# Kernel tuning notes

Hardware: AMD Instinct MI355X
Metric: run time of the kernel (lower is better)

The kernel has to match this reference:

```python
import jax, jax.numpy as jnp
import numpy as np
import math

B, L, D, H = 8, 2048, 1024, 1024


def setup_inputs() -> dict:
    key = jax.random.key(0)
    ks = jax.random.split(key, 6)
    scale = 1.0 / math.sqrt(D)
    return {
        "input_q": jax.random.normal(ks[0], (B, L, D), dtype=jnp.float32),
        "input_k": jax.random.normal(ks[1], (B, L, D), dtype=jnp.float32),
        "k_mask": jax.random.uniform(ks[2], (B, L), dtype=jnp.float32),
        "Wq": jax.random.normal(ks[3], (D, H), dtype=jnp.float32) * scale,
        "bq": jnp.zeros((H,), dtype=jnp.float32),
        "Wk": jax.random.normal(ks[4], (D, H), dtype=jnp.float32) * scale,
        "bk": jnp.zeros((H,), dtype=jnp.float32),
    }


def reference(input_q, input_k, k_mask, Wq, bq, Wk, bk):
    # Linear projections: (b, l, d) @ (d, h) -> (b, l, h)
    q = input_q @ Wq + bq
    k = input_k @ Wk + bk
    # Faithful to original: mask values become 0.0 or -1e9, then an
    # outer product bmm((b,l,1),(b,1,l)) builds the (b,l,l) additive mask.
    m = jnp.where(k_mask > 0.5, 0.0, -1000000000.0)  # (b, l)
    add_mask = m[:, :, None] * m[:, None, :]          # (b, l, l) outer product
    # Scaled dot-product scores
    attn = jnp.einsum("bqh,bkh->bqk", q, k) / math.sqrt(H)
    attn = jax.nn.softmax(attn + add_mask, axis=-1)
    # Weighted sum over the ORIGINAL input_k (not projected k), as in source
    out = jnp.einsum("bqk,bkd->bqd", attn, input_k)
    return out
```

## Files before the change

kernel.cpp:

```cpp
#include <hip/hip_runtime.h>

#define BATCH 8
#define SEQ   2048
#define DIM   1024

typedef __attribute__((ext_vector_type(8)))  short short8;
typedef __attribute__((ext_vector_type(4)))  short short4v;
typedef __attribute__((ext_vector_type(4)))  float floatx4;
typedef __attribute__((ext_vector_type(16))) float floatx16;

__device__ __forceinline__ unsigned short f32_to_bf16(float f) {
    union { float f; unsigned int u; } x; x.f = f;
    unsigned int r = x.u + 0x7fffu + ((x.u >> 16) & 1u);
    return (unsigned short)(r >> 16);
}

__device__ __forceinline__ float bf16_to_f32(unsigned short h) {
    union { unsigned int u; float f; } x; x.u = ((unsigned int)h) << 16;
    return x.f;
}

__device__ __forceinline__ void async_load16(const void* g, void* l) {
    __builtin_amdgcn_global_load_lds(
        (const __attribute__((address_space(1))) void*)g,
        (__attribute__((address_space(3))) void*)l, 16, 0, 0);
}

__global__ __launch_bounds__(256) void build_idx(
    const float* __restrict__ mask, int* __restrict__ idx,
    int* __restrict__ cnt, int* __restrict__ padcnt)
{
    const int b = blockIdx.x;
    const int t = threadIdx.x;
    const float* mb = mask + b * SEQ;
    int flags[8]; int c = 0;
#pragma unroll
    for (int j = 0; j < 8; ++j) {
        flags[j] = (mb[t * 8 + j] > 0.5f) ? 1 : 0;
        c += flags[j];
    }
    int sc = c;
    for (int o = 1; o < 64; o <<= 1) {
        int v = __shfl_up(sc, o);
        if ((t & 63) >= o) sc += v;
    }
    __shared__ int wtot[4];
    const int lane = t & 63, wave = t >> 6;
    if (lane == 63) wtot[wave] = sc;
    __syncthreads();
    int woff = 0;
    for (int w = 0; w < wave; ++w) woff += wtot[w];
    int p = woff + sc - c;
#pragma unroll
    for (int j = 0; j < 8; ++j)
        if (flags[j]) idx[b * SEQ + (p++)] = t * 8 + j;
    __syncthreads();
    const int total = wtot[0] + wtot[1] + wtot[2] + wtot[3];
    if (t == 0) { cnt[b] = total; padcnt[b] = (total + 127) & ~127; }
    for (int q = total + t; q < SEQ; q += 256) idx[b * SEQ + q] = 0;
}

__global__ __launch_bounds__(256) void gather_cvt_q(
    const float* __restrict__ xq, const int* __restrict__ idx,
    const int* __restrict__ padcnt, unsigned short* __restrict__ qc)
{
    const int b = blockIdx.y;
    const int rc = blockIdx.x;
    if (rc >= padcnt[b]) return;
    const int src = idx[b * SEQ + rc];
    const float* s = xq + ((long)b * SEQ + src) * DIM + threadIdx.x * 4;
    unsigned short* d = qc + ((long)b * SEQ + rc) * DIM + threadIdx.x * 4;
    floatx4 v = *(const floatx4*)s;
    short4v w;
#pragma unroll
    for (int j = 0; j < 4; ++j) w[j] = (short)f32_to_bf16(v[j]);
    *(short4v*)d = w;
}

__global__ __launch_bounds__(256) void prep_kv(
    const float* __restrict__ xk, const float* __restrict__ mask,
    unsigned short* __restrict__ kbf, unsigned short* __restrict__ Vt,
    float* __restrict__ mavg)
{
    __shared__ float tile[32][33];
    __shared__ float msk[32];
    __shared__ float csum[8][32];
    const int b  = blockIdx.z;
    const int c0 = blockIdx.x * 32;
    const int r0 = blockIdx.y * 32;
    const int tx = threadIdx.x & 31, ty = threadIdx.x >> 5;
    const float* xb = xk + (long)b * SEQ * DIM;
    unsigned short* kb = kbf + (long)b * SEQ * DIM;
    unsigned short* vb = Vt + (long)b * DIM * SEQ;

    if (threadIdx.x < 32) msk[threadIdx.x] = mask[b * SEQ + r0 + threadIdx.x];

    float v[4];
#pragma unroll
    for (int i = 0; i < 4; ++i) {
        const int r = ty + i * 8;
        v[i] = xb[(long)(r0 + r) * DIM + c0 + tx];
        tile[r][tx] = v[i];
        kb[(long)(r0 + r) * DIM + c0 + tx] = f32_to_bf16(v[i]);
    }
    __syncthreads();

    float s = 0.f;
#pragma unroll
    for (int i = 0; i < 4; ++i) {
        const int r = ty + i * 8;
        s += (msk[r] <= 0.5f) ? v[i] : 0.f;
    }
    csum[ty][tx] = s;

#pragma unroll
    for (int i = 0; i < 4; ++i) {
        const int c = ty + i * 8;
        vb[(long)(c0 + c) * SEQ + r0 + tx] = f32_to_bf16(tile[tx][c]);
    }
    __syncthreads();
    if (ty == 0) {
        float t = 0.f;
#pragma unroll
        for (int j = 0; j < 8; ++j) t += csum[j][tx];
        atomicAdd(&mavg[b * DIM + c0 + tx], t);
    }
}

__global__ __launch_bounds__(256) void cvt_bf16(
    const float* __restrict__ src, unsigned short* __restrict__ dst)
{
    const long i = ((long)blockIdx.x * 256 + threadIdx.x) * 8;
    floatx4 v0 = *(const floatx4*)(src + i);
    floatx4 v1 = *(const floatx4*)(src + i + 4);
    short8 w;
#pragma unroll
    for (int j = 0; j < 4; ++j) w[j]     = (short)f32_to_bf16(v0[j]);
#pragma unroll
    for (int j = 0; j < 4; ++j) w[4 + j] = (short)f32_to_bf16(v1[j]);
    *(short8*)(dst + i) = w;
}

__global__ __launch_bounds__(256) void proj_bias(
    const float* __restrict__ bq, const float* __restrict__ Wk, float* __restrict__ g0)
{
    const int n = blockIdx.x;
    const int t = threadIdx.x;
    float s = 0.f;
    for (int h = t; h < DIM; h += 256) s += bq[h] * Wk[(long)n * DIM + h];
    for (int o = 32; o; o >>= 1) s += __shfl_xor(s, o);
    __shared__ float r[4];
    if ((t & 63) == 0) r[t >> 6] = s;
    __syncthreads();
    if (t == 0) g0[n] = r[0] + r[1] + r[2] + r[3];
}

template<bool C_BF16, bool BIAS, bool LIMIT, bool SCATTER, int FLAT>
__global__ __launch_bounds__(256) void gemm_bt(
    const unsigned short* __restrict__ A, const unsigned short* __restrict__ Bt,
    void* __restrict__ Cp, const float* __restrict__ bias,
    int N, int K, long sA, long sB, long sC, float scale,
    const int* __restrict__ mlim, const int* __restrict__ cntp,
    const int* __restrict__ idx, int sh)
{
    int bx, by, bz;
    if (FLAT == 0) {
        bx = blockIdx.x; by = blockIdx.y; bz = blockIdx.z;
    } else {
        const int id = blockIdx.x;
        bz = id & 7;
        const int rem = id >> 3;
        const int m = (1 << sh) - 1;
        if (FLAT == 1) { bx = rem & m; by = rem >> sh; }
        else           { by = rem & m; bx = rem >> sh; }
    }
    const int row0 = bx * 128;
    if (LIMIT && row0 >= mlim[bz]) return;

    __shared__ unsigned short As[128 * 64];
    __shared__ unsigned short Bs[128 * 64];

    const int tid  = threadIdx.x;
    const int lane = tid & 63;
    const int wave = tid >> 6;
    const int wm   = wave >> 1;
    const int wn   = wave & 1;
    const int l31  = lane & 31;
    const int half = lane >> 5;
    const int x7   = lane & 7;
    const int col0 = by * 128;
    const long zA = (long)bz * sA;
    const long zB = (long)bz * sB;
    const long zC = (long)bz * sC;

    const int sr = lane >> 3;
    const int sq = ((lane & 7) ^ sr) * 8;

    const unsigned short* Abase = A  + zA + (long)row0 * K;
    const unsigned short* Bbase = Bt + zB + (long)col0 * K;
    const unsigned short* aptr[4];
    const unsigned short* bptr[4];
#pragma unroll
    for (int c = 0; c < 4; ++c) {
        const int r = (wave * 4 + c) * 8 + sr;
        aptr[c] = Abase + (long)r * K + sq;
        bptr[c] = Bbase + (long)r * K + sq;
    }

    floatx16 acc[2][2];
#pragma unroll
    for (int a = 0; a < 2; ++a)
#pragma unroll
        for (int b = 0; b < 2; ++b)
#pragma unroll
            for (int r = 0; r < 16; ++r) acc[a][b][r] = 0.f;

    const int raf[2] = { (wm * 64 +  0 + l31) * 64, (wm * 64 + 32 + l31) * 64 };
    const int rbf[2] = { (wn * 64 +  0 + l31) * 64, (wn * 64 + 32 + l31) * 64 };

    for (int kt = 0; kt < K; kt += 64) {
#pragma unroll
        for (int c = 0; c < 4; ++c) {
            const int chunk = wave * 4 + c;
            async_load16(aptr[c] + kt, As + chunk * 512);
            async_load16(bptr[c] + kt, Bs + chunk * 512);
        }
        __syncthreads();

#pragma unroll
        for (int ks = 0; ks < 4; ++ks) {
            const int sw = ((ks * 2 + half) ^ x7) << 3;
            short8 af[2], bf[2];
#pragma unroll
            for (int t = 0; t < 2; ++t) {
                af[t] = *(const short8*)(As + raf[t] + sw);
                bf[t] = *(const short8*)(Bs + rbf[t] + sw);
            }
#pragma unroll
            for (int tm = 0; tm < 2; ++tm)
#pragma unroll
                for (int tn = 0; tn < 2; ++tn)
                    acc[tm][tn] = __builtin_amdgcn_mfma_f32_32x32x16_bf16(
                        af[tm], bf[tn], acc[tm][tn], 0, 0, 0);
        }
        __syncthreads();
    }

    const int climit = SCATTER ? cntp[bz] : 0;
    const int* ridx  = SCATTER ? (idx + bz * SEQ) : (const int*)nullptr;
#pragma unroll
    for (int tn = 0; tn < 2; ++tn) {
        const int ccol = col0 + wn * 64 + tn * 32 + l31;
        float bv = 0.f;
        if (BIAS) bv = bias[ccol];
#pragma unroll
        for (int tm = 0; tm < 2; ++tm) {
            const int rbase = row0 + wm * 64 + tm * 32 + 4 * half;
#pragma unroll
            for (int r = 0; r < 16; ++r) {
                const int crow = rbase + (r & 3) + 8 * (r >> 2);
                float v = acc[tm][tn][r] * scale + bv;
                long orow = crow;
                if (SCATTER) {
                    if (crow >= climit) continue;
                    orow = ridx[crow];
                }
                const long ci = zC + orow * (long)N + ccol;
                if (C_BF16) ((unsigned short*)Cp)[ci] = f32_to_bf16(v);
                else        ((float*)Cp)[ci] = v;
            }
        }
    }
}

__global__ __launch_bounds__(256) void softmax_rows(
    unsigned short* __restrict__ S, const int* __restrict__ padcnt)
{
    const int b = blockIdx.x >> 11, rc = blockIdx.x & 2047;
    if (rc >= padcnt[b]) return;
    const long base = (long)blockIdx.x * SEQ + threadIdx.x * 8;
    const int lane = threadIdx.x & 63, wave = threadIdx.x >> 6;
    __shared__ float rbuf[8];

    short8 v = *(const short8*)(S + base);
    float x[8];
#pragma unroll
    for (int j = 0; j < 8; ++j) x[j] = bf16_to_f32((unsigned short)v[j]);

    float m = x[0];
#pragma unroll
    for (int j = 1; j < 8; ++j) m = fmaxf(m, x[j]);
    for (int o = 32; o; o >>= 1) m = fmaxf(m, __shfl_xor(m, o));
    if (lane == 0) rbuf[wave] = m;
    __syncthreads();
    m = fmaxf(fmaxf(rbuf[0], rbuf[1]), fmaxf(rbuf[2], rbuf[3]));

    float e[8], s = 0.f;
#pragma unroll
    for (int j = 0; j < 8; ++j) { e[j] = __expf(x[j] - m); s += e[j]; }
    for (int o = 32; o; o >>= 1) s += __shfl_xor(s, o);
    if (lane == 0) rbuf[4 + wave] = s;
    __syncthreads();
    s = rbuf[4] + rbuf[5] + rbuf[6] + rbuf[7];
    const float inv = 1.0f / s;

    short8 o8;
#pragma unroll
    for (int j = 0; j < 8; ++j) o8[j] = (short)f32_to_bf16(e[j] * inv);
    *(short8*)(S + base) = o8;
}

__global__ __launch_bounds__(256) void overwrite_masked(
    float* __restrict__ out, const float* __restrict__ mask,
    const float* __restrict__ mavg, const int* __restrict__ cnt)
{
    const int bid = blockIdx.x;
    const int b = bid >> 11;
    if (mask[bid] > 0.5f) return;
    const float inv = 1.0f / (float)(SEQ - cnt[b]);
    const long obase = (long)bid * DIM;
    const float* mv = mavg + b * DIM;
    for (int d = threadIdx.x; d < DIM; d += 256)
        out[obase + d] = mv[d] * inv;
}

extern "C" void kernel_launch(void* const* d_in, const int* in_sizes, int n_in,
                              void* d_out, int out_size, void* d_ws, size_t ws_size,
                              hipStream_t stream) {
    (void)in_sizes; (void)n_in; (void)out_size;
    const float* input_q = (const float*)d_in[0];
    const float* input_k = (const float*)d_in[1];
    const float* k_mask  = (const float*)d_in[2];
    const float* Wq      = (const float*)d_in[3];
    const float* bq      = (const float*)d_in[4];
    const float* Wk      = (const float*)d_in[5];
    const float* bk      = (const float*)d_in[6];
    (void)bk;
    float* out = (float*)d_out;

    char* ws = (char*)d_ws;
    unsigned short* qc   = (unsigned short*)(ws);
    unsigned short* S    = (unsigned short*)(ws);
    unsigned short* qpp  = (unsigned short*)(ws + 67108864);
    unsigned short* Wqb  = (unsigned short*)(ws + 67108864);
    unsigned short* Wkb  = (unsigned short*)(ws + 69206016);
    unsigned short* kbf  = (unsigned short*)(ws + 100663296);
    unsigned short* Vt   = (unsigned short*)(ws + 134217728);
    unsigned short* Gt   = (unsigned short*)(ws + 167772160);
    float*          g0   = (float*)(ws + 169869312);
    float*          mavg = (float*)(ws + 169873408);
    int*            idx  = (int*)(ws + 169906176);
    int*            cnts = (int*)(ws + 169971712);
    int*            pcnt = (int*)(ws + 169971744);
    if (ws_size < 169971776) return;

    hipMemsetAsync(mavg, 0, BATCH * DIM * sizeof(float), stream);

    build_idx<<<BATCH, 256, 0, stream>>>(k_mask, idx, cnts, pcnt);
    gather_cvt_q<<<dim3(SEQ, BATCH), 256, 0, stream>>>(input_q, idx, pcnt, qc);
    prep_kv<<<dim3(DIM / 32, SEQ / 32, BATCH), 256, 0, stream>>>(input_k, k_mask, kbf, Vt, mavg);
    cvt_bf16<<<512, 256, 0, stream>>>(Wq, Wqb);
    cvt_bf16<<<512, 256, 0, stream>>>(Wk, Wkb);
    proj_bias<<<DIM, 256, 0, stream>>>(bq, Wk, g0);

    gemm_bt<true, false, false, false, 0><<<dim3(8, 8, 1), 256, 0, stream>>>(
        Wkb, Wqb, Gt, nullptr, DIM, DIM, 0, 0, 0, 1.0f, nullptr, nullptr, nullptr, 0);

    gemm_bt<true, true, true, false, 2><<<8 * 16 * 8, 256, 0, stream>>>(
        qc, Gt, qpp, g0, DIM, DIM,
        (long)SEQ * DIM, 0, (long)SEQ * DIM, 1.0f, pcnt, nullptr, nullptr, 3);

    gemm_bt<true, false, true, false, 1><<<8 * 16 * 16, 256, 0, stream>>>(
        qpp, kbf, S, nullptr, SEQ, DIM,
        (long)SEQ * DIM, (long)SEQ * DIM, (long)SEQ * SEQ, 0.03125f, pcnt, nullptr, nullptr, 4);

    softmax_rows<<<BATCH * SEQ, 256, 0, stream>>>(S, pcnt);

    gemm_bt<false, false, true, true, 2><<<8 * 16 * 8, 256, 0, stream>>>(
        S, Vt, out, nullptr, DIM, SEQ,
        (long)SEQ * SEQ, (long)DIM * SEQ, (long)SEQ * DIM, 1.0f, pcnt, cnts, idx, 3);

    overwrite_masked<<<BATCH * SEQ, 256, 0, stream>>>(out, k_mask, mavg, cnts);
}
```

Baseline: 365.5 us.

## Double-buffer GEMM LDS tiles with async prefetch two stages ahead

Turns the single-buffer GEMM main loop into a two-slot LDS ping-pong. The global-to-LDS load for tile t+2 is issued right after the last fragment reads of tile t, and waits use explicit vmcnt/lgkmcnt counts with raw s_barrier instead of __syncthreads, so global latency overlaps with MFMA work. MFMA bursts run at raised wave priority via s_setprio. LDS use doubles to 64 KB per block, which may lower occupancy, and the hand-written waitcnt values must match the issued load count exactly.

Measured after the change: 401.5 us. 1.1x slower.

```diff
diff --git a/kernel.cpp b/kernel.cpp
--- a/kernel.cpp
+++ b/kernel.cpp
@@ -177,8 +177,8 @@
     const int row0 = bx * 128;
     if (LIMIT && row0 >= mlim[bz]) return;
 
-    __shared__ unsigned short As[128 * 64];
-    __shared__ unsigned short Bs[128 * 64];
+    __shared__ unsigned short As[2][128 * 64];
+    __shared__ unsigned short Bs[2][128 * 64];
 
     const int tid  = threadIdx.x;
     const int lane = tid & 63;
@@ -207,6 +207,15 @@
         bptr[c] = Bbase + (long)r * K + sq;
     }
 
+    auto stage = [&](int slot, int ktElem) {
+#pragma unroll
+        for (int c = 0; c < 4; ++c) {
+            const int chunk = wave * 4 + c;
+            async_load16(aptr[c] + ktElem, &As[slot][chunk * 512]);
+            async_load16(bptr[c] + ktElem, &Bs[slot][chunk * 512]);
+        }
+    };
+
     floatx16 acc[2][2];
 #pragma unroll
     for (int a = 0; a < 2; ++a)
@@ -218,32 +227,80 @@
     const int raf[2] = { (wm * 64 +  0 + l31) * 64, (wm * 64 + 32 + l31) * 64 };
     const int rbf[2] = { (wn * 64 +  0 + l31) * 64, (wn * 64 + 32 + l31) * 64 };
 
-    for (int kt = 0; kt < K; kt += 64) {
-#pragma unroll
-        for (int c = 0; c < 4; ++c) {
-            const int chunk = wave * 4 + c;
-            async_load16(aptr[c] + kt, As + chunk * 512);
-            async_load16(bptr[c] + kt, Bs + chunk * 512);
+    const int NT = K >> 6;
+
+    stage(0, 0);
+    if (NT > 1) {
+        stage(1, 64);
+        asm volatile("s_waitcnt vmcnt(8)" ::: "memory");
+    } else {
+        asm volatile("s_waitcnt vmcnt(0)" ::: "memory");
+    }
+    __builtin_amdgcn_sched_barrier(0);
+    __builtin_amdgcn_s_barrier();
+    __builtin_amdgcn_sched_barrier(0);
+
+    for (int t = 0; t < NT; ++t) {
+        const int cur = t & 1;
+        const unsigned short* Ac = &As[cur][0];
+        const unsigned short* Bc = &Bs[cur][0];
+
+        short8 af[2][2], bf[2][2];
+#pragma unroll
+        for (int ks = 0; ks < 2; ++ks) {
+            const int sw = ((ks * 2 + half) ^ x7) << 3;
+#pragma unroll
+            for (int tt = 0; tt < 2; ++tt) {
+                af[ks][tt] = *(const short8*)(Ac + raf[tt] + sw);
+                bf[ks][tt] = *(const short8*)(Bc + rbf[tt] + sw);
+            }
         }
-        __syncthreads();
-
-#pragma unroll
-        for (int ks = 0; ks < 4; ++ks) {
-            const int sw = ((ks * 2 + half) ^ x7) << 3;
-            short8 af[2], bf[2];
-#pragma unroll
-            for (int t = 0; t < 2; ++t) {
-                af[t] = *(const short8*)(As + raf[t] + sw);
-                bf[t] = *(const short8*)(Bs + rbf[t] + sw);
-            }
+        asm volatile("s_waitcnt lgkmcnt(0)" ::: "memory");
+        __builtin_amdgcn_sched_barrier(0);
+        __builtin_amdgcn_s_setprio(1);
+#pragma unroll
+        for (int ks = 0; ks < 2; ++ks)
 #pragma unroll
             for (int tm = 0; tm < 2; ++tm)
 #pragma unroll
                 for (int tn = 0; tn < 2; ++tn)
                     acc[tm][tn] = __builtin_amdgcn_mfma_f32_32x32x16_bf16(
-                        af[tm], bf[tn], acc[tm][tn], 0, 0, 0);
+                        af[ks][tm], bf[ks][tn], acc[tm][tn], 0, 0, 0);
+        __builtin_amdgcn_s_setprio(0);
+
+#pragma unroll
+        for (int ks = 0; ks < 2; ++ks) {
+            const int sw = (((ks + 2) * 2 + half) ^ x7) << 3;
+#pragma unroll
+            for (int tt = 0; tt < 2; ++tt) {
+                af[ks][tt] = *(const short8*)(Ac + raf[tt] + sw);
+                bf[ks][tt] = *(const short8*)(Bc + rbf[tt] + sw);
+            }
         }
-        __syncthreads();
+        asm volatile("s_waitcnt lgkmcnt(0)" ::: "memory");
+        __builtin_amdgcn_sched_barrier(0);
+        __builtin_amdgcn_s_barrier();
+        __builtin_amdgcn_sched_barrier(0);
+        if (t + 2 < NT) stage(cur, (t + 2) * 64);
+        __builtin_amdgcn_sched_barrier(0);
+        __builtin_amdgcn_s_setprio(1);
+#pragma unroll
+        for (int ks = 0; ks < 2; ++ks)
+#pragma unroll
+            for (int tm = 0; tm < 2; ++tm)
+#pragma unroll
+                for (int tn = 0; tn < 2; ++tn)
+                    acc[tm][tn] = __builtin_amdgcn_mfma_f32_32x32x16_bf16(
+                        af[ks][tm], bf[ks][tn], acc[tm][tn], 0, 0, 0);
+        __builtin_amdgcn_s_setprio(0);
+
+        if (t + 1 < NT) {
+            if (t + 2 < NT) asm volatile("s_waitcnt vmcnt(8)" ::: "memory");
+            else            asm volatile("s_waitcnt vmcnt(0)" ::: "memory");
+            __builtin_amdgcn_sched_barrier(0);
+            __builtin_amdgcn_s_barrier();
+            __builtin_amdgcn_sched_barrier(0);
+        }
     }
 
     const int climit = SCATTER ? cntp[bz] : 0;
```

## Add 256x256-tile 8-wave GEMM with double-buffered LDS ping-pong schedule

Applied to the files above, without the earlier changes.

Introduces a new gemm256 kernel using 256x256 output tiles, 512 threads, 128KB dynamic LDS with double buffering and a fine-grained barrier-interleaved schedule of LDS reads, async global-to-LDS loads and 16x16x32 bf16 MFMAs. The three large batched GEMMs (q projection, scores, and attention-times-V) switch from the 128-tile gemm_bt to this kernel. The aim is more data reuse per tile and better overlap of memory traffic with MFMA work. In exchange, grids are much smaller, so there are fewer blocks to spread across CUs, one block per CU because of LDS usage, and wave quantization and masked-row limits may leave CUs idle.

Result: slower. 401.7 us (+9.9%).

```diff
diff --git a/kernel.cpp b/kernel.cpp
--- a/kernel.cpp
+++ b/kernel.cpp
@@ -25,6 +25,11 @@
         (const __attribute__((address_space(1))) void*)g,
         (__attribute__((address_space(3))) void*)l, 16, 0, 0);
 }
+
+#define CFENCE asm volatile("" ::: "memory")
+#define BARF() do { CFENCE; __builtin_amdgcn_s_barrier(); CFENCE; } while (0)
+#define WAIT_LGKM0 do { asm volatile("s_waitcnt lgkmcnt(0)" ::: "memory"); \
+                        __builtin_amdgcn_sched_barrier(0); } while (0)
 
 __global__ __launch_bounds__(256) void build_idx(
     const float* __restrict__ mask, int* __restrict__ idx,
@@ -260,6 +265,232 @@
             for (int r = 0; r < 16; ++r) {
                 const int crow = rbase + (r & 3) + 8 * (r >> 2);
                 float v = acc[tm][tn][r] * scale + bv;
+                long orow = crow;
+                if (SCATTER) {
+                    if (crow >= climit) continue;
+                    orow = ridx[crow];
+                }
+                const long ci = zC + orow * (long)N + ccol;
+                if (C_BF16) ((unsigned short*)Cp)[ci] = f32_to_bf16(v);
+                else        ((float*)Cp)[ci] = v;
+            }
+        }
+    }
+}
+
+template<int D, int MQ>
+__device__ __forceinline__ void read_a256(short8 (&af)[4][2],
+                                          const unsigned short* const (&aB)[2][2]) {
+#pragma unroll
+    for (int mm = 0; mm < 4; ++mm)
+#pragma unroll
+        for (int ss = 0; ss < 2; ++ss)
+            af[mm][ss] = *(const short8*)(aB[D][ss] + (MQ * 64 + mm * 16) * 64);
+}
+
+template<int D, int NQ>
+__device__ __forceinline__ void read_b256(short8 (&bf)[2][2][2],
+                                          const unsigned short* const (&bB)[2][2]) {
+#pragma unroll
+    for (int nn = 0; nn < 2; ++nn)
+#pragma unroll
+        for (int ss = 0; ss < 2; ++ss)
+            bf[NQ][nn][ss] = *(const short8*)(bB[D][ss] + (NQ * 32 + nn * 16) * 64);
+}
+
+template<int MQ, int NQ>
+__device__ __forceinline__ void mfma_q256(floatx4 (&acc)[8][4],
+                                          const short8 (&af)[4][2],
+                                          const short8 (&bf)[2][2][2]) {
+    __builtin_amdgcn_s_setprio(1);
+#pragma unroll
+    for (int mm = 0; mm < 4; ++mm)
+#pragma unroll
+        for (int nn = 0; nn < 2; ++nn)
+#pragma unroll
+            for (int ss = 0; ss < 2; ++ss)
+                acc[MQ * 4 + mm][NQ * 2 + nn] = __builtin_amdgcn_mfma_f32_16x16x32_bf16(
+                    af[mm][ss], bf[NQ][nn][ss], acc[MQ * 4 + mm][NQ * 2 + nn], 0, 0, 0);
+    __builtin_amdgcn_s_setprio(0);
+}
+
+__device__ __forceinline__ void stage2(const unsigned short* s0, const unsigned short* s1,
+                                       unsigned short* d) {
+    async_load16(s0, d);
+    async_load16(s1, d + 512);
+}
+
+template<bool C_BF16, bool BIAS, bool LIMIT, bool SCATTER, int FLAT>
+__global__ __launch_bounds__(512) void gemm256(
+    const unsigned short* __restrict__ A, const unsigned short* __restrict__ Bt,
+    void* __restrict__ Cp, const float* __restrict__ bias,
+    int N, int K, long sA, long sB, long sC, float scale,
+    const int* __restrict__ mlim, const int* __restrict__ cntp,
+    const int* __restrict__ idx, int sh)
+{
+    extern __shared__ unsigned short smem[];
+    unsigned short* AsP = smem;
+    unsigned short* BsP = smem + 32768;
+
+    int bx, by, bz;
+    if (FLAT == 0) {
+        bx = blockIdx.x; by = blockIdx.y; bz = blockIdx.z;
+    } else {
+        const int id = blockIdx.x;
+        bz = id & 7;
+        const int rem = id >> 3;
+        const int m = (1 << sh) - 1;
+        if (FLAT == 1) { bx = rem & m; by = rem >> sh; }
+        else           { by = rem & m; bx = rem >> sh; }
+    }
+    const int row0 = bx * 256;
+    if (LIMIT && row0 >= mlim[bz]) return;
+    const int col0 = by * 256;
+
+    const int tid  = threadIdx.x;
+    const int lane = tid & 63;
+    const int wave = tid >> 6;
+    const int wm   = wave >> 2;
+    const int wn   = wave & 3;
+    const int l15  = lane & 15;
+    const int kg   = lane >> 4;
+    const int l7   = lane & 7;
+    const long zA = (long)bz * sA;
+    const long zB = (long)bz * sB;
+    const long zC = (long)bz * sC;
+
+    const int sr = lane >> 3;
+    const int sq = ((lane & 7) ^ sr) * 8;
+    const unsigned short* Abase = A  + zA + (long)row0 * K;
+    const unsigned short* Bbase = Bt + zB + (long)col0 * K;
+    const unsigned short* aSrc[2][2];
+    const unsigned short* bSrc[2][2];
+#pragma unroll
+    for (int h = 0; h < 2; ++h)
+#pragma unroll
+        for (int cc = 0; cc < 2; ++cc) {
+            const long r = h * 128 + wave * 16 + cc * 8 + sr;
+            aSrc[h][cc] = Abase + r * K + sq;
+            bSrc[h][cc] = Bbase + r * K + sq;
+        }
+
+    const int sOff0 = ((0 * 4 + kg) ^ l7) * 8;
+    const int sOff1 = ((1 * 4 + kg) ^ l7) * 8;
+    const unsigned short* aB[2][2];
+    const unsigned short* bB[2][2];
+#pragma unroll
+    for (int d = 0; d < 2; ++d) {
+        aB[d][0] = AsP + (d * 2 + wm) * 8192 + l15 * 64 + sOff0;
+        aB[d][1] = AsP + (d * 2 + wm) * 8192 + l15 * 64 + sOff1;
+        bB[d][0] = BsP + (d * 2 + (wn >> 1)) * 8192 + ((wn & 1) * 64 + l15) * 64 + sOff0;
+        bB[d][1] = BsP + (d * 2 + (wn >> 1)) * 8192 + ((wn & 1) * 64 + l15) * 64 + sOff1;
+    }
+
+    floatx4 acc[8][4];
+#pragma unroll
+    for (int mm = 0; mm < 8; ++mm)
+#pragma unroll
+        for (int nn = 0; nn < 4; ++nn)
+#pragma unroll
+            for (int r = 0; r < 4; ++r) acc[mm][nn][r] = 0.f;
+
+    short8 af[4][2];
+    short8 bf[2][2][2];
+
+#define ST_A(DD, HH, KT) stage2(aSrc[HH][0] + (KT), aSrc[HH][1] + (KT), \
+                                AsP + ((DD) * 2 + (HH)) * 8192 + wave * 1024)
+#define ST_B(DD, HH, KT) stage2(bSrc[HH][0] + (KT), bSrc[HH][1] + (KT), \
+                                BsP + ((DD) * 2 + (HH)) * 8192 + wave * 1024)
+
+    const int NI = K >> 7;
+
+    ST_B(0, 0, 0);  ST_B(0, 1, 0);
+    ST_A(0, 0, 0);  ST_A(0, 1, 0);
+    ST_B(1, 0, 64); ST_B(1, 1, 64);
+    asm volatile("s_waitcnt vmcnt(4)" ::: "memory");
+    __builtin_amdgcn_sched_barrier(0);
+    BARF();
+
+#pragma unroll 1
+    for (int i = 0; i < NI; ++i) {
+        const bool nl = (i < NI - 1);
+        const long kA = (long)(2 * i + 1) * 64;
+        const long kB = (long)(2 * i + 2) * 64;
+        const long kC = (long)(2 * i + 3) * 64;
+
+        read_a256<0, 0>(af, aB);
+        read_b256<0, 0>(bf, bB);
+        ST_A(1, 0, kA);
+        asm volatile("s_waitcnt lgkmcnt(8)" ::: "memory");
+        BARF();
+        WAIT_LGKM0;
+        mfma_q256<0, 0>(acc, af, bf);
+        BARF();
+        read_b256<0, 1>(bf, bB);
+        ST_A(1, 1, kA);
+        BARF();
+        WAIT_LGKM0;
+        mfma_q256<0, 1>(acc, af, bf);
+        BARF();
+        read_a256<0, 1>(af, aB);
+        if (nl) ST_B(0, 0, kB);
+        BARF();
+        WAIT_LGKM0;
+        mfma_q256<1, 1>(acc, af, bf);
+        BARF();
+        if (nl) ST_B(0, 1, kB);
+        BARF();
+        mfma_q256<1, 0>(acc, af, bf);
+        if (nl) { asm volatile("s_waitcnt vmcnt(4)" ::: "memory"); }
+        else    { asm volatile("s_waitcnt vmcnt(0)" ::: "memory"); }
+        __builtin_amdgcn_sched_barrier(0);
+        BARF();
+        read_a256<1, 0>(af, aB);
+        read_b256<1, 0>(bf, bB);
+        if (nl) ST_A(0, 0, kB);
+        asm volatile("s_waitcnt lgkmcnt(8)" ::: "memory");
+        BARF();
+        WAIT_LGKM0;
+        mfma_q256<0, 0>(acc, af, bf);
+        BARF();
+        read_b256<1, 1>(bf, bB);
+        if (nl) ST_A(0, 1, kB);
+        BARF();
+        WAIT_LGKM0;
+        mfma_q256<0, 1>(acc, af, bf);
+        BARF();
+        read_a256<1, 1>(af, aB);
+        if (nl) ST_B(1, 0, kC);
+        BARF();
+        WAIT_LGKM0;
+        mfma_q256<1, 1>(acc, af, bf);
+        BARF();
+        if (nl) ST_B(1, 1, kC);
+        BARF();
+        mfma_q256<1, 0>(acc, af, bf);
+        if (nl) {
+            asm volatile("s_waitcnt vmcnt(4)" ::: "memory");
+            __builtin_amdgcn_sched_barrier(0);
+            BARF();
+        }
+    }
+#undef ST_A
+#undef ST_B
+
+    const int climit = SCATTER ? cntp[bz] : 0;
+    const int* ridx  = SCATTER ? (idx + bz * SEQ) : (const int*)nullptr;
+#pragma unroll
+    for (int nn = 0; nn < 4; ++nn) {
+        const int ccol = col0 + wn * 64 + nn * 16 + l15;
+        float bv = 0.f;
+        if (BIAS) bv = bias[ccol];
+#pragma unroll
+        for (int mm = 0; mm < 8; ++mm) {
+            const int rb = row0 + wm * 128 + mm * 16 + kg * 4;
+#pragma unroll
+            for (int r = 0; r < 4; ++r) {
+                const int crow = rb + r;
+                float v = acc[mm][nn][r] * scale + bv;
                 long orow = crow;
                 if (SCATTER) {
                     if (crow >= climit) continue;
@@ -354,6 +585,17 @@
     int*            pcnt = (int*)(ws + 169971744);
     if (ws_size < 169971776) return;
 
+    static bool attr_set = false;
+    if (!attr_set) {
+        hipFuncSetAttribute((const void*)gemm256<true, true, true, false, 2>,
+                            hipFuncAttributeMaxDynamicSharedMemorySize, 131072);
+        hipFuncSetAttribute((const void*)gemm256<true, false, true, false, 1>,
+                            hipFuncAttributeMaxDynamicSharedMemorySize, 131072);
+        hipFuncSetAttribute((const void*)gemm256<false, false, true, true, 2>,
+                            hipFuncAttributeMaxDynamicSharedMemorySize, 131072);
+        attr_set = true;
+    }
+
     hipMemsetAsync(mavg, 0, BATCH * DIM * sizeof(float), stream);
 
     build_idx<<<BATCH, 256, 0, stream>>>(k_mask, idx, cnts, pcnt);
@@ -366,19 +608,19 @@
     gemm_bt<true, false, false, false, 0><<<dim3(8, 8, 1), 256, 0, stream>>>(
         Wkb, Wqb, Gt, nullptr, DIM, DIM, 0, 0, 0, 1.0f, nullptr, nullptr, nullptr, 0);
 
-    gemm_bt<true, true, true, false, 2><<<8 * 16 * 8, 256, 0, stream>>>(
+    gemm256<true, true, true, false, 2><<<8 * 8 * 4, 512, 131072, stream>>>(
         qc, Gt, qpp, g0, DIM, DIM,
-        (long)SEQ * DIM, 0, (long)SEQ * DIM, 1.0f, pcnt, nullptr, nullptr, 3);
-
-    gemm_bt<true, false, true, false, 1><<<8 * 16 * 16, 256, 0, stream>>>(
+        (long)SEQ * DIM, 0, (long)SEQ * DIM, 1.0f, pcnt, nullptr, nullptr, 2);
+
+    gemm256<true, false, true, false, 1><<<8 * 8 * 8, 512, 131072, stream>>>(
         qpp, kbf, S, nullptr, SEQ, DIM,
-        (long)SEQ * DIM, (long)SEQ * DIM, (long)SEQ * SEQ, 0.03125f, pcnt, nullptr, nullptr, 4);
+        (long)SEQ * DIM, (long)SEQ * DIM, (long)SEQ * SEQ, 0.03125f, pcnt, nullptr, nullptr, 3);
 
     softmax_rows<<<BATCH * SEQ, 256, 0, stream>>>(S, pcnt);
 
-    gemm_bt<false, false, true, true, 2><<<8 * 16 * 8, 256, 0, stream>>>(
+    gemm256<false, false, true, true, 2><<<8 * 8 * 4, 512, 131072, stream>>>(
         S, Vt, out, nullptr, DIM, SEQ,
-        (long)SEQ * SEQ, (long)DIM * SEQ, (long)SEQ * DIM, 1.0f, pcnt, cnts, idx, 3);
+        (long)SEQ * SEQ, (long)DIM * SEQ, (long)SEQ * DIM, 1.0f, pcnt, cnts, idx, 2);
 
     overwrite_masked<<<BATCH * SEQ, 256, 0, stream>>>(out, k_mask, mavg, cnts);
 }
```
